# Performance work log

Measured on AMD Instinct MI355X. Metric: run time of the kernel, lower is better.

## Reference

```python
import jax, jax.numpy as jnp
import numpy as np

LOG_2PI = float(np.log(2.0 * np.pi))


def setup_inputs() -> dict:
    key = jax.random.key(0)
    k1, k2 = jax.random.split(key)
    M, N, D = 8192, 16384, 16
    x_eval = jax.random.normal(k1, (M, D), dtype=jnp.float32)
    x_base = jax.random.normal(k2, (N, D), dtype=jnp.float32)
    # module stores log_bw = log(bw_init); use log(0.2)
    log_bw = jnp.full((1,), np.log(0.2), dtype=jnp.float32)
    return {"x_eval": x_eval, "x_base": x_base, "log_bw": log_bw}


def reference(x_eval, x_base, log_bw):
    N = x_base.shape[0]
    D = x_base.shape[1]
    bw2 = jnp.exp(2.0 * log_bw)  # bw ** 2, shape [1]
    # pairwise squared distances [M, N] via the gemm-based expansion
    sq_e = jnp.sum(x_eval * x_eval, axis=1, keepdims=True)          # [M, 1]
    sq_b = jnp.sum(x_base * x_base, axis=1, keepdims=True).T        # [1, N]
    cross = jnp.einsum('md,nd->mn', x_eval, x_base)                 # [M, N]
    d2 = sq_e + sq_b - 2.0 * cross                                  # [M, N]
    t2 = -0.5 * d2 / bw2                                            # log Gaussian kernel
    t1 = -0.5 * D * LOG_2PI - log_bw                                # scalar-ish [1]
    val = jnp.exp(t1 + t2).sum(axis=1) / N                          # [M]
    return val
```

## Files before the change

### kernel.cpp

```cpp
#include <hip/hip_runtime.h>
#include <math.h>


#define LOG_2PI_F 1.8378770664093453f
#define LOG2E_F   1.4426950408889634f

#define M_PTS 8192
#define N_PTS 16384

typedef __attribute__((ext_vector_type(8)))  short bf16x8;
typedef __attribute__((ext_vector_type(16))) float f32x16;

static __device__ __forceinline__ unsigned short f2bf(float x) {
    unsigned u = __float_as_uint(x);
    u += 0x7fffu + ((u >> 16) & 1u);
    return (unsigned short)(u >> 16);
}
static __device__ __forceinline__ float bf2f(unsigned short h) {
    return __uint_as_float(((unsigned)h) << 16);
}
static __device__ __forceinline__ uint4 pack8(const unsigned short* a) {
    uint4 u;
    u.x = (unsigned)a[0] | ((unsigned)a[1] << 16);
    u.y = (unsigned)a[2] | ((unsigned)a[3] << 16);
    u.z = (unsigned)a[4] | ((unsigned)a[5] << 16);
    u.w = (unsigned)a[6] | ((unsigned)a[7] << 16);
    return u;
}

__global__ __launch_bounds__(256) void kde_pack(
        const float* __restrict__ x, int rows, int is_eval,
        unsigned short* __restrict__ ph, unsigned short* __restrict__ pl,
        unsigned short* __restrict__ pn) {
    int r = blockIdx.x * 256 + threadIdx.x;
    if (r >= rows) return;
    const float4* row = (const float4*)(x + (size_t)r * 16);
    unsigned short hs[16], ls[16], ns[16];
    float s = 0.f;
#pragma unroll
    for (int k = 0; k < 4; ++k) {
        float4 v = row[k];
        float c0 = v.x, c1 = v.y, c2 = v.z, c3 = v.w;
        unsigned short h;
        h = f2bf(c0); hs[k*4+0] = h; ls[k*4+0] = f2bf(c0 - bf2f(h)); s = fmaf(c0, c0, s);
        h = f2bf(c1); hs[k*4+1] = h; ls[k*4+1] = f2bf(c1 - bf2f(h)); s = fmaf(c1, c1, s);
        h = f2bf(c2); hs[k*4+2] = h; ls[k*4+2] = f2bf(c2 - bf2f(h)); s = fmaf(c2, c2, s);
        h = f2bf(c3); hs[k*4+3] = h; ls[k*4+3] = f2bf(c3 - bf2f(h)); s = fmaf(c3, c3, s);
    }
    float cb = -0.5f * s;
    unsigned short ch = f2bf(cb);
    unsigned short cl = f2bf(cb - bf2f(ch));
#pragma unroll
    for (int i = 0; i < 16; ++i) ns[i] = 0;
    if (is_eval) { ns[0] = 0x3F80; ns[1] = 0x3F80; ns[2] = ch;     ns[3] = cl; }
    else         { ns[0] = ch;     ns[1] = cl;     ns[2] = 0x3F80; ns[3] = 0x3F80; }

    uint4* dh = (uint4*)(ph + (size_t)r * 16);
    uint4* dl = (uint4*)(pl + (size_t)r * 16);
    uint4* dn = (uint4*)(pn + (size_t)r * 16);
    dh[0] = pack8(hs); dh[1] = pack8(hs + 8);
    dl[0] = pack8(ls); dl[1] = pack8(ls + 8);
    dn[0] = pack8(ns); dn[1] = pack8(ns + 8);
}

__global__ __launch_bounds__(256) void kde_mfma(
        const unsigned short* __restrict__ eh, const unsigned short* __restrict__ el,
        const unsigned short* __restrict__ en,
        const unsigned short* __restrict__ bh, const unsigned short* __restrict__ bl,
        const unsigned short* __restrict__ bn,
        const float* __restrict__ log_bw, float* __restrict__ part) {
    const int lane = threadIdx.x & 63;
    const int w = blockIdx.x * 4 + (threadIdx.x >> 6);
    const int chunk = w >> 7;
    const int etp   = w & 127;
    const int col   = lane & 31;
    const int kg    = lane >> 5;

    const float k2l = __expf(-2.f * log_bw[0]) * LOG2E_F;

    size_t e0 = ((size_t)etp * 64 + col) * 16 + (size_t)kg * 8;
    size_t e1 = e0 + 32 * 16;
    const bf16x8 Bh0 = *(const bf16x8*)(eh + e0);
    const bf16x8 Bl0 = *(const bf16x8*)(el + e0);
    const bf16x8 Bn0 = *(const bf16x8*)(en + e0);
    const bf16x8 Bh1 = *(const bf16x8*)(eh + e1);
    const bf16x8 Bl1 = *(const bf16x8*)(el + e1);
    const bf16x8 Bn1 = *(const bf16x8*)(en + e1);

    size_t aoff = ((size_t)chunk * 512 + col) * 16 + (size_t)kg * 8;
    const unsigned short* pah = bh + aoff;
    const unsigned short* pal = bl + aoff;
    const unsigned short* pan = bn + aoff;

    float a00 = 0.f, a01 = 0.f, a10 = 0.f, a11 = 0.f;

    for (int t = 0; t < 16; ++t) {
        const bf16x8 Ah = *(const bf16x8*)pah;
        const bf16x8 Al = *(const bf16x8*)pal;
        const bf16x8 An = *(const bf16x8*)pan;
        pah += 32 * 16; pal += 32 * 16; pan += 32 * 16;

        f32x16 C0, C1;
#pragma unroll
        for (int r = 0; r < 16; ++r) { C0[r] = 0.f; C1[r] = 0.f; }
        C0 = __builtin_amdgcn_mfma_f32_32x32x16_bf16(Ah, Bh0, C0, 0, 0, 0);
        C0 = __builtin_amdgcn_mfma_f32_32x32x16_bf16(Ah, Bl0, C0, 0, 0, 0);
        C0 = __builtin_amdgcn_mfma_f32_32x32x16_bf16(Al, Bh0, C0, 0, 0, 0);
        C0 = __builtin_amdgcn_mfma_f32_32x32x16_bf16(An, Bn0, C0, 0, 0, 0);
        C1 = __builtin_amdgcn_mfma_f32_32x32x16_bf16(Ah, Bh1, C1, 0, 0, 0);
        C1 = __builtin_amdgcn_mfma_f32_32x32x16_bf16(Ah, Bl1, C1, 0, 0, 0);
        C1 = __builtin_amdgcn_mfma_f32_32x32x16_bf16(Al, Bh1, C1, 0, 0, 0);
        C1 = __builtin_amdgcn_mfma_f32_32x32x16_bf16(An, Bn1, C1, 0, 0, 0);

#pragma unroll
        for (int r = 0; r < 16; r += 2) {
            a00 += __builtin_amdgcn_exp2f(C0[r]     * k2l);
            a01 += __builtin_amdgcn_exp2f(C0[r + 1] * k2l);
            a10 += __builtin_amdgcn_exp2f(C1[r]     * k2l);
            a11 += __builtin_amdgcn_exp2f(C1[r + 1] * k2l);
        }
    }

    float s0 = a00 + a01;
    float s1 = a10 + a11;
    s0 += __shfl_xor(s0, 32, 64);
    s1 += __shfl_xor(s1, 32, 64);
    if (lane < 32) {
        float* p = part + (size_t)chunk * M_PTS + (size_t)etp * 64;
        p[col]      = s0;
        p[32 + col] = s1;
    }
}

__global__ __launch_bounds__(256) void kde_reduce(
        const float* __restrict__ part, const float* __restrict__ log_bw,
        float* __restrict__ out) {
    int m = blockIdx.x * 256 + threadIdx.x;
    if (m >= M_PTS) return;
    float lb = log_bw[0];
    float scale = __expf(-8.f * LOG_2PI_F - lb) / (float)N_PTS;
    float s = 0.f;
#pragma unroll
    for (int c = 0; c < 32; ++c) s += part[(size_t)c * M_PTS + m];
    out[m] = scale * s;
}

extern "C" void kernel_launch(void* const* d_in, const int* in_sizes, int n_in,
                              void* d_out, int out_size, void* d_ws, size_t ws_size,
                              hipStream_t stream) {
    const float* xe = (const float*)d_in[0];
    const float* xb = (const float*)d_in[1];
    const float* lb = (const float*)d_in[2];
    float* out = (float*)d_out;

    unsigned short* w0 = (unsigned short*)d_ws;
    unsigned short* bh = w0;
    unsigned short* bl = bh + (size_t)N_PTS * 16;
    unsigned short* bn = bl + (size_t)N_PTS * 16;
    unsigned short* eh = bn + (size_t)N_PTS * 16;
    unsigned short* el = eh + (size_t)M_PTS * 16;
    unsigned short* en = el + (size_t)M_PTS * 16;
    float* part = (float*)(en + (size_t)M_PTS * 16);

    kde_pack<<<N_PTS / 256, 256, 0, stream>>>(xb, N_PTS, 0, bh, bl, bn);
    kde_pack<<<M_PTS / 256, 256, 0, stream>>>(xe, M_PTS, 1, eh, el, en);
    kde_mfma<<<1024, 256, 0, stream>>>(eh, el, en, bh, bl, bn, lb, part);
    kde_reduce<<<M_PTS / 256, 256, 0, stream>>>(part, lb, out);
}
```

Baseline: 51.34 us.

## Fold bandwidth scale into packed operands, merge pack launches, regrid MFMA work

Pre-scales the eval operands and the norm terms by the log2e/bw^2 factor during packing. The exp2 can then take the MFMA output directly and skips a multiply per element. The two pack launches become one kernel. The MFMA kernel now gives each wave one 32-column eval tile instead of two, splits the base points into 64 chunks, fully unrolls the inner loop, and launches 4096 blocks with an occupancy hint. The added parallelism and lower register pressure come at the cost of less reuse of each base-point load, more partial sums to reduce, and some precision risk from splitting the pre-scaled values into bf16 hi/lo parts.

```diff
diff --git a/kernel.cpp b/kernel.cpp
--- a/kernel.cpp
+++ b/kernel.cpp
@@ -7,6 +7,9 @@
 
 #define M_PTS 8192
 #define N_PTS 16384
+#define NCH   64
+#define ROWS_PER_CHUNK (N_PTS / NCH)
+#define TPC (ROWS_PER_CHUNK / 32)
 
 typedef __attribute__((ext_vector_type(8)))  short bf16x8;
 typedef __attribute__((ext_vector_type(16))) float f32x16;
@@ -29,107 +32,108 @@
 }
 
 __global__ __launch_bounds__(256) void kde_pack(
-        const float* __restrict__ x, int rows, int is_eval,
-        unsigned short* __restrict__ ph, unsigned short* __restrict__ pl,
-        unsigned short* __restrict__ pn) {
+        const float* __restrict__ xe, const float* __restrict__ xb,
+        const float* __restrict__ log_bw,
+        unsigned short* __restrict__ bh, unsigned short* __restrict__ bl,
+        unsigned short* __restrict__ bn,
+        unsigned short* __restrict__ eh, unsigned short* __restrict__ el,
+        unsigned short* __restrict__ en) {
     int r = blockIdx.x * 256 + threadIdx.x;
-    if (r >= rows) return;
-    const float4* row = (const float4*)(x + (size_t)r * 16);
+    if (r >= N_PTS + M_PTS) return;
+    const float k2l = __expf(-2.f * log_bw[0]) * LOG2E_F;
+
+    int is_eval = (r >= N_PTS);
+    int rr = is_eval ? (r - N_PTS) : r;
+    const float* src = is_eval ? xe : xb;
+    float dscale = is_eval ? k2l : 1.0f;
+
+    const float4* row = (const float4*)(src + (size_t)rr * 16);
     unsigned short hs[16], ls[16], ns[16];
     float s = 0.f;
 #pragma unroll
     for (int k = 0; k < 4; ++k) {
         float4 v = row[k];
-        float c0 = v.x, c1 = v.y, c2 = v.z, c3 = v.w;
-        unsigned short h;
-        h = f2bf(c0); hs[k*4+0] = h; ls[k*4+0] = f2bf(c0 - bf2f(h)); s = fmaf(c0, c0, s);
-        h = f2bf(c1); hs[k*4+1] = h; ls[k*4+1] = f2bf(c1 - bf2f(h)); s = fmaf(c1, c1, s);
-        h = f2bf(c2); hs[k*4+2] = h; ls[k*4+2] = f2bf(c2 - bf2f(h)); s = fmaf(c2, c2, s);
-        h = f2bf(c3); hs[k*4+3] = h; ls[k*4+3] = f2bf(c3 - bf2f(h)); s = fmaf(c3, c3, s);
+        float c[4] = {v.x, v.y, v.z, v.w};
+#pragma unroll
+        for (int j = 0; j < 4; ++j) {
+            s = fmaf(c[j], c[j], s);
+            float d = c[j] * dscale;
+            unsigned short h = f2bf(d);
+            hs[k*4+j] = h;
+            ls[k*4+j] = f2bf(d - bf2f(h));
+        }
     }
-    float cb = -0.5f * s;
-    unsigned short ch = f2bf(cb);
-    unsigned short cl = f2bf(cb - bf2f(ch));
+    float cn = -0.5f * s * k2l;
+    unsigned short ch = f2bf(cn);
+    unsigned short cl = f2bf(cn - bf2f(ch));
 #pragma unroll
     for (int i = 0; i < 16; ++i) ns[i] = 0;
     if (is_eval) { ns[0] = 0x3F80; ns[1] = 0x3F80; ns[2] = ch;     ns[3] = cl; }
     else         { ns[0] = ch;     ns[1] = cl;     ns[2] = 0x3F80; ns[3] = 0x3F80; }
 
-    uint4* dh = (uint4*)(ph + (size_t)r * 16);
-    uint4* dl = (uint4*)(pl + (size_t)r * 16);
-    uint4* dn = (uint4*)(pn + (size_t)r * 16);
+    unsigned short* ph = is_eval ? eh : bh;
+    unsigned short* pl = is_eval ? el : bl;
+    unsigned short* pn = is_eval ? en : bn;
+    uint4* dh = (uint4*)(ph + (size_t)rr * 16);
+    uint4* dl = (uint4*)(pl + (size_t)rr * 16);
+    uint4* dn = (uint4*)(pn + (size_t)rr * 16);
     dh[0] = pack8(hs); dh[1] = pack8(hs + 8);
     dl[0] = pack8(ls); dl[1] = pack8(ls + 8);
     dn[0] = pack8(ns); dn[1] = pack8(ns + 8);
 }
 
-__global__ __launch_bounds__(256) void kde_mfma(
+__global__ __launch_bounds__(256, 8) void kde_mfma(
         const unsigned short* __restrict__ eh, const unsigned short* __restrict__ el,
         const unsigned short* __restrict__ en,
         const unsigned short* __restrict__ bh, const unsigned short* __restrict__ bl,
         const unsigned short* __restrict__ bn,
-        const float* __restrict__ log_bw, float* __restrict__ part) {
+        float* __restrict__ part) {
     const int lane = threadIdx.x & 63;
-    const int w = blockIdx.x * 4 + (threadIdx.x >> 6);
-    const int chunk = w >> 7;
-    const int etp   = w & 127;
-    const int col   = lane & 31;
-    const int kg    = lane >> 5;
+    const int widx = threadIdx.x >> 6;
+    const int b = blockIdx.x;
+    const int chunk = b >> 6;
+    const int etp = (b & 63) * 4 + widx;
+    const int col = lane & 31;
+    const int kg  = lane >> 5;
 
-    const float k2l = __expf(-2.f * log_bw[0]) * LOG2E_F;
+    const size_t eoff = ((size_t)etp * 32 + col) * 16 + (size_t)kg * 8;
+    const bf16x8 Bh = *(const bf16x8*)(eh + eoff);
+    const bf16x8 Bl = *(const bf16x8*)(el + eoff);
+    const bf16x8 Bn = *(const bf16x8*)(en + eoff);
 
-    size_t e0 = ((size_t)etp * 64 + col) * 16 + (size_t)kg * 8;
-    size_t e1 = e0 + 32 * 16;
-    const bf16x8 Bh0 = *(const bf16x8*)(eh + e0);
-    const bf16x8 Bl0 = *(const bf16x8*)(el + e0);
-    const bf16x8 Bn0 = *(const bf16x8*)(en + e0);
-    const bf16x8 Bh1 = *(const bf16x8*)(eh + e1);
-    const bf16x8 Bl1 = *(const bf16x8*)(el + e1);
-    const bf16x8 Bn1 = *(const bf16x8*)(en + e1);
-
-    size_t aoff = ((size_t)chunk * 512 + col) * 16 + (size_t)kg * 8;
+    size_t aoff = ((size_t)chunk * ROWS_PER_CHUNK + col) * 16 + (size_t)kg * 8;
     const unsigned short* pah = bh + aoff;
     const unsigned short* pal = bl + aoff;
     const unsigned short* pan = bn + aoff;
 
-    float a00 = 0.f, a01 = 0.f, a10 = 0.f, a11 = 0.f;
+    float acc0 = 0.f, acc1 = 0.f;
 
-    for (int t = 0; t < 16; ++t) {
+#pragma unroll
+    for (int t = 0; t < TPC; ++t) {
         const bf16x8 Ah = *(const bf16x8*)pah;
         const bf16x8 Al = *(const bf16x8*)pal;
         const bf16x8 An = *(const bf16x8*)pan;
         pah += 32 * 16; pal += 32 * 16; pan += 32 * 16;
 
-        f32x16 C0, C1;
+        f32x16 C;
 #pragma unroll
-        for (int r = 0; r < 16; ++r) { C0[r] = 0.f; C1[r] = 0.f; }
-        C0 = __builtin_amdgcn_mfma_f32_32x32x16_bf16(Ah, Bh0, C0, 0, 0, 0);
-        C0 = __builtin_amdgcn_mfma_f32_32x32x16_bf16(Ah, Bl0, C0, 0, 0, 0);
-        C0 = __builtin_amdgcn_mfma_f32_32x32x16_bf16(Al, Bh0, C0, 0, 0, 0);
-        C0 = __builtin_amdgcn_mfma_f32_32x32x16_bf16(An, Bn0, C0, 0, 0, 0);
-        C1 = __builtin_amdgcn_mfma_f32_32x32x16_bf16(Ah, Bh1, C1, 0, 0, 0);
-        C1 = __builtin_amdgcn_mfma_f32_32x32x16_bf16(Ah, Bl1, C1, 0, 0, 0);
-        C1 = __builtin_amdgcn_mfma_f32_32x32x16_bf16(Al, Bh1, C1, 0, 0, 0);
-        C1 = __builtin_amdgcn_mfma_f32_32x32x16_bf16(An, Bn1, C1, 0, 0, 0);
+        for (int r = 0; r < 16; ++r) C[r] = 0.f;
+        C = __builtin_amdgcn_mfma_f32_32x32x16_bf16(Ah, Bh, C, 0, 0, 0);
+        C = __builtin_amdgcn_mfma_f32_32x32x16_bf16(Ah, Bl, C, 0, 0, 0);
+        C = __builtin_amdgcn_mfma_f32_32x32x16_bf16(Al, Bh, C, 0, 0, 0);
+        C = __builtin_amdgcn_mfma_f32_32x32x16_bf16(An, Bn, C, 0, 0, 0);
 
 #pragma unroll
         for (int r = 0; r < 16; r += 2) {
-            a00 += __builtin_amdgcn_exp2f(C0[r]     * k2l);
-            a01 += __builtin_amdgcn_exp2f(C0[r + 1] * k2l);
-            a10 += __builtin_amdgcn_exp2f(C1[r]     * k2l);
-            a11 += __builtin_amdgcn_exp2f(C1[r + 1] * k2l);
+            acc0 += __builtin_amdgcn_exp2f(C[r]);
+            acc1 += __builtin_amdgcn_exp2f(C[r + 1]);
         }
     }
 
-    float s0 = a00 + a01;
-    float s1 = a10 + a11;
-    s0 += __shfl_xor(s0, 32, 64);
-    s1 += __shfl_xor(s1, 32, 64);
-    if (lane < 32) {
-        float* p = part + (size_t)chunk * M_PTS + (size_t)etp * 64;
-        p[col]      = s0;
-        p[32 + col] = s1;
-    }
+    float s = acc0 + acc1;
+    s += __shfl_xor(s, 32, 64);
+    if (lane < 32)
+        part[(size_t)chunk * M_PTS + (size_t)etp * 32 + col] = s;
 }
 
 __global__ __launch_bounds__(256) void kde_reduce(
@@ -141,7 +145,7 @@
     float scale = __expf(-8.f * LOG_2PI_F - lb) / (float)N_PTS;
     float s = 0.f;
 #pragma unroll
-    for (int c = 0; c < 32; ++c) s += part[(size_t)c * M_PTS + m];
+    for (int c = 0; c < NCH; ++c) s += part[(size_t)c * M_PTS + m];
     out[m] = scale * s;
 }
 
@@ -153,8 +157,7 @@
     const float* lb = (const float*)d_in[2];
     float* out = (float*)d_out;
 
-    unsigned short* w0 = (unsigned short*)d_ws;
-    unsigned short* bh = w0;
+    unsigned short* bh = (unsigned short*)d_ws;
     unsigned short* bl = bh + (size_t)N_PTS * 16;
     unsigned short* bn = bl + (size_t)N_PTS * 16;
     unsigned short* eh = bn + (size_t)N_PTS * 16;
@@ -162,8 +165,8 @@
     unsigned short* en = el + (size_t)M_PTS * 16;
     float* part = (float*)(en + (size_t)M_PTS * 16);
 
-    kde_pack<<<N_PTS / 256, 256, 0, stream>>>(xb, N_PTS, 0, bh, bl, bn);
-    kde_pack<<<M_PTS / 256, 256, 0, stream>>>(xe, M_PTS, 1, eh, el, en);
-    kde_mfma<<<1024, 256, 0, stream>>>(eh, el, en, bh, bl, bn, lb, part);
+    kde_pack<<<(N_PTS + M_PTS) / 256, 256, 0, stream>>>(xe, xb, lb,
+                                                        bh, bl, bn, eh, el, en);
+    kde_mfma<<<4096, 256, 0, stream>>>(eh, el, en, bh, bl, bn, part);
     kde_reduce<<<M_PTS / 256, 256, 0, stream>>>(part, lb, out);
 }
```

After: 47.68 us. 1.08x faster.
